# Optimization experiments

Hardware: AMD Instinct MI355X
Metric: run time of the kernel (lower is better)

The kernel has to match this reference:

```python
import jax, jax.numpy as jnp
import numpy as np

D_MODEL = 1024
NUM_HEADS = 16
D_K = D_MODEL // NUM_HEADS


def setup_inputs() -> dict:
    key = jax.random.key(0)
    ks = jax.random.split(key, 9)
    B, S = 2, 2048
    s = 1.0 / np.sqrt(D_MODEL)
    return {
        "x": jax.random.normal(ks[0], (B, S, D_MODEL), dtype=jnp.float32),
        "Wq": jax.random.normal(ks[1], (D_MODEL, D_MODEL), dtype=jnp.float32) * s,
        "bq": jnp.zeros((D_MODEL,), dtype=jnp.float32),
        "Wk": jax.random.normal(ks[2], (D_MODEL, D_MODEL), dtype=jnp.float32) * s,
        "bk": jnp.zeros((D_MODEL,), dtype=jnp.float32),
        "Wv": jax.random.normal(ks[3], (D_MODEL, D_MODEL), dtype=jnp.float32) * s,
        "bv": jnp.zeros((D_MODEL,), dtype=jnp.float32),
        "Wo": jax.random.normal(ks[4], (D_MODEL, D_MODEL), dtype=jnp.float32) * s,
        "bo": jnp.zeros((D_MODEL,), dtype=jnp.float32),
    }


def reference(x, Wq, bq, Wk, bk, Wv, bv, Wo, bo):
    B, S, _ = x.shape
    # project and split heads: [B, H, S, d_k]
    def proj(W, b):
        return (x @ W + b).reshape(B, S, NUM_HEADS, D_K).transpose(0, 2, 1, 3)
    Q, K, V = proj(Wq, bq), proj(Wk, bk), proj(Wv, bv)
    scores = jnp.einsum("bhqd,bhkd->bhqk", Q, K) / jnp.sqrt(jnp.float32(D_K))
    causal = jnp.tril(jnp.ones((S, S), dtype=bool))
    scores = jnp.where(causal[None, None], scores, jnp.float32(-1e9))
    attn = jax.nn.softmax(scores, axis=-1)  # dropout=0 (eval)
    out = jnp.einsum("bhqk,bhkd->bhqd", attn, V)
    out = out.transpose(0, 2, 1, 3).reshape(B, S, D_MODEL)
    return out @ Wo + bo
```

## Files before the change

kernel.cpp:

```cpp
#include <hip/hip_runtime.h>

#define SEQ    2048
#define NH     16
#define DMODEL 1024

typedef __attribute__((ext_vector_type(4)))  float f32x4;
typedef __attribute__((ext_vector_type(8)))  short s16x8;
typedef __attribute__((ext_vector_type(4)))  short s16x4;
typedef __attribute__((ext_vector_type(2)))  unsigned u32x2;

__device__ __forceinline__ float bf2f(unsigned short u){
  union { unsigned int i; float f; } v; v.i = ((unsigned int)u) << 16; return v.f;
}
__device__ __forceinline__ unsigned short f2bf(float f){
  union { float f; unsigned int i; } v; v.f = f;
  unsigned int r = v.i + 0x7fffu + ((v.i >> 16) & 1u);
  return (unsigned short)(r >> 16);
}
__device__ __forceinline__ unsigned short f2bf_hu(float f){
  union { float f; unsigned int i; } v; v.f = f;
  return (unsigned short)((v.i + 0x8000u) >> 16);
}
__device__ __forceinline__ float fast_exp2(float x){
  return __builtin_amdgcn_exp2f(x);
}
__device__ __forceinline__ void gld_lds16(const void* g, void* l){
  __builtin_amdgcn_global_load_lds((const __attribute__((address_space(1))) void*)g,
                                   (__attribute__((address_space(3))) void*)l,
                                   16, 0, 0);
}
#define SB() __builtin_amdgcn_sched_barrier(0)

__global__ __launch_bounds__(256) void k_prep(const float* __restrict__ x,
                                              const float* __restrict__ W0,
                                              const float* __restrict__ W1,
                                              const float* __restrict__ W2,
                                              const float* __restrict__ W3,
                                              unsigned short* __restrict__ Wt,
                                              unsigned short* __restrict__ xh){
  __shared__ float t[64][65];
  const int bid = blockIdx.x;
  const int tid = threadIdx.x;
  if (bid < 1024){
    const int z = bid >> 8, rem = bid & 255;
    const int n0 = (rem & 15) * 64, k0 = (rem >> 4) * 64;
    const float* Ws[4] = {W0, W1, W2, W3};
    const float* W = Ws[z];
    #pragma unroll
    for (int i = 0; i < 16; ++i){
      int e = i * 256 + tid;
      int r = e >> 6, c = e & 63;
      t[r][c] = W[(size_t)(k0 + r) * 1024 + n0 + c];
    }
    __syncthreads();
    size_t base = ((size_t)z << 20);
    #pragma unroll
    for (int i = 0; i < 16; ++i){
      int e = i * 256 + tid;
      int nn = e >> 6, kk = e & 63;
      Wt[base + (size_t)(n0 + nn) * 1024 + k0 + kk] = f2bf(t[kk][nn]);
    }
  } else {
    int i = (bid - 1024) * 256 + tid;
    f32x4 v = ((const f32x4*)x)[i];
    s16x4 h;
    #pragma unroll
    for (int j = 0; j < 4; ++j) h[j] = (short)f2bf(v[j]);
    ((s16x4*)xh)[i] = h;
  }
}

__global__ __launch_bounds__(512, 2)
void gemm_qkv8(const unsigned short* __restrict__ A,
               const unsigned short* __restrict__ B,
               const float* __restrict__ bq, const float* __restrict__ bk,
               const float* __restrict__ bv,
               unsigned short* __restrict__ Qb, unsigned short* __restrict__ Kb,
               unsigned short* __restrict__ Vt)
{
  __shared__ __align__(16) unsigned short lA[2][256 * 64];
  __shared__ __align__(16) unsigned short lB[2][192 * 64];
  const int tid = threadIdx.x;
  const int lane = tid & 63, w = tid >> 6;
  const int wm = w >> 2, wn = w & 3;
  const int lr = lane & 15, lq = lane >> 4;
  const int wg  = blockIdx.x + blockIdx.y * 16;
  const int swz = (wg & 7) * 32 + (wg >> 3);
  const int m0 = (swz >> 4) * 256, n0 = (swz & 15) * 192;

  size_t asrc[4]; unsigned adst[4];
  #pragma unroll
  for (int p = 0; p < 4; ++p){
    int c = p * 512 + tid;
    int row = c >> 3, lc = (c & 7) ^ (row & 7);
    asrc[p] = (size_t)(m0 + row) * 1024 + lc * 8;
    adst[p] = c * 8;
  }
  size_t bsrc[3]; unsigned bdst[3];
  #pragma unroll
  for (int p = 0; p < 3; ++p){
    int c = p * 512 + tid;
    int row = c >> 3, lc = (c & 7) ^ (row & 7);
    bsrc[p] = (size_t)(n0 + row) * 1024 + lc * 8;
    bdst[p] = c * 8;
  }
  auto stage = [&](int buf, int k0){
    #pragma unroll
    for (int p = 0; p < 4; ++p) gld_lds16(A + asrc[p] + k0, &lA[buf][adst[p]]);
    #pragma unroll
    for (int p = 0; p < 3; ++p) gld_lds16(B + bsrc[p] + k0, &lB[buf][bdst[p]]);
  };

  const int csw0 = ((0 + lq) ^ (lr & 7)) << 4;
  const int csw1 = ((4 + lq) ^ (lr & 7)) << 4;

  f32x4 acc[8][3];
  #pragma unroll
  for (int i = 0; i < 8; ++i)
    #pragma unroll
    for (int j = 0; j < 3; ++j) acc[i][j] = (f32x4)0.0f;

  stage(0, 0);
  stage(1, 64);
  asm volatile("s_waitcnt vmcnt(7)" ::: "memory");
  SB();
  __builtin_amdgcn_s_barrier();
  SB();

  for (int t = 0; t < 16; ++t){
    const int p = t & 1;
    s16x8 fa[8][2], fb[3][2];
    const char* baseA = (const char*)&lA[p][0];
    const char* baseB = (const char*)&lB[p][0];
    #pragma unroll
    for (int mf = 0; mf < 8; ++mf)
      fa[mf][0] = *(const s16x8*)(baseA + (wm * 128 + mf * 16 + lr) * 128 + csw0);
    #pragma unroll
    for (int nf = 0; nf < 3; ++nf)
      fb[nf][0] = *(const s16x8*)(baseB + (wn * 48 + nf * 16 + lr) * 128 + csw0);
    SB();
    #pragma unroll
    for (int mf = 0; mf < 8; ++mf)
      fa[mf][1] = *(const s16x8*)(baseA + (wm * 128 + mf * 16 + lr) * 128 + csw1);
    #pragma unroll
    for (int nf = 0; nf < 3; ++nf)
      fb[nf][1] = *(const s16x8*)(baseB + (wn * 48 + nf * 16 + lr) * 128 + csw1);
    asm volatile("s_waitcnt lgkmcnt(11)" ::: "memory");
    SB();
    #pragma unroll
    for (int mf = 0; mf < 8; ++mf)
      #pragma unroll
      for (int nf = 0; nf < 3; ++nf)
        acc[mf][nf] = __builtin_amdgcn_mfma_f32_16x16x32_bf16(fa[mf][0], fb[nf][0], acc[mf][nf], 0, 0, 0);
    SB();
    asm volatile("s_waitcnt lgkmcnt(0)" ::: "memory");
    SB();
    __builtin_amdgcn_s_barrier();
    SB();
    if (t + 2 < 16) stage(p, (t + 2) * 64);
    #pragma unroll
    for (int mf = 0; mf < 8; ++mf)
      #pragma unroll
      for (int nf = 0; nf < 3; ++nf)
        acc[mf][nf] = __builtin_amdgcn_mfma_f32_16x16x32_bf16(fa[mf][1], fb[nf][1], acc[mf][nf], 0, 0, 0);
    SB();
    if (t < 14) asm volatile("s_waitcnt vmcnt(7)" ::: "memory");
    else        asm volatile("s_waitcnt vmcnt(0)" ::: "memory");
    SB();
    __builtin_amdgcn_s_barrier();
    SB();
  }

  const int mb = m0 + wm * 128, nb = n0 + wn * 48;
  #pragma unroll
  for (int mf = 0; mf < 8; ++mf){
    int row = mb + mf * 16 + lq * 4;
    #pragma unroll
    for (int nf = 0; nf < 3; ++nf){
      int col = nb + nf * 16 + lr;
      int mat = col >> 10, cm = col & 1023;
      float bs = ((mat == 0) ? bq : (mat == 1) ? bk : bv)[cm];
      if (mat < 2){
        unsigned short* QK = mat ? Kb : Qb;
        #pragma unroll
        for (int r = 0; r < 4; ++r)
          QK[(size_t)(row + r) * 1024 + cm] = f2bf(acc[mf][nf][r] + bs);
      } else {
        int bb = row >> 11, s = row & 2047;
        int h = cm >> 6, d = cm & 63;
        s16x4 pk;
        #pragma unroll
        for (int r = 0; r < 4; ++r) pk[r] = (short)f2bf(acc[mf][nf][r] + bs);
        *(s16x4*)&Vt[(((size_t)(bb * NH + h) * 64 + d) << 11) + s] = pk;
      }
    }
  }
}

__global__ __launch_bounds__(256, 2)
void gemm_o8(const unsigned short* __restrict__ A,
             const unsigned short* __restrict__ B,
             const float* __restrict__ bias,
             float* __restrict__ C)
{
  __shared__ __align__(16) unsigned short lA[2][64 * 64];
  __shared__ __align__(16) unsigned short lB[2][128 * 64];
  const int tid = threadIdx.x;
  const int lane = tid & 63, w = tid >> 6;
  const int wm = w >> 1, wn = w & 1;
  const int lr = lane & 15, lq = lane >> 4;
  const int wg  = blockIdx.x + blockIdx.y * 8;
  const int swz = (wg & 7) * 64 + (wg >> 3);
  const int m0 = (swz >> 3) * 64, n0 = (swz & 7) * 128;

  size_t asrc[2]; unsigned adst[2];
  #pragma unroll
  for (int p = 0; p < 2; ++p){
    int c = p * 256 + tid;
    int row = c >> 3, lc = (c & 7) ^ (row & 7);
    asrc[p] = (size_t)(m0 + row) * 1024 + lc * 8;
    adst[p] = c * 8;
  }
  size_t bsrc[4]; unsigned bdst[4];
  #pragma unroll
  for (int p = 0; p < 4; ++p){
    int c = p * 256 + tid;
    int row = c >> 3, lc = (c & 7) ^ (row & 7);
    bsrc[p] = (size_t)(n0 + row) * 1024 + lc * 8;
    bdst[p] = c * 8;
  }
  auto stage = [&](int buf, int k0){
    #pragma unroll
    for (int p = 0; p < 2; ++p) gld_lds16(A + asrc[p] + k0, &lA[buf][adst[p]]);
    #pragma unroll
    for (int p = 0; p < 4; ++p) gld_lds16(B + bsrc[p] + k0, &lB[buf][bdst[p]]);
  };

  const int csw0 = ((0 + lq) ^ (lr & 7)) << 4;
  const int csw1 = ((4 + lq) ^ (lr & 7)) << 4;

  f32x4 acc[2][4];
  #pragma unroll
  for (int i = 0; i < 2; ++i)
    #pragma unroll
    for (int j = 0; j < 4; ++j) acc[i][j] = (f32x4)0.0f;

  stage(0, 0);
  stage(1, 64);
  asm volatile("s_waitcnt vmcnt(6)" ::: "memory");
  SB();
  __builtin_amdgcn_s_barrier();
  SB();

  for (int t = 0; t < 16; ++t){
    const int p = t & 1;
    s16x8 fa[2][2], fb[4][2];
    const char* baseA = (const char*)&lA[p][0];
    const char* baseB = (const char*)&lB[p][0];
    #pragma unroll
    for (int mf = 0; mf < 2; ++mf)
      fa[mf][0] = *(const s16x8*)(baseA + (wm * 32 + mf * 16 + lr) * 128 + csw0);
    #pragma unroll
    for (int nf = 0; nf < 4; ++nf)
      fb[nf][0] = *(const s16x8*)(baseB + (wn * 64 + nf * 16 + lr) * 128 + csw0);
    SB();
    #pragma unroll
    for (int mf = 0; mf < 2; ++mf)
      fa[mf][1] = *(const s16x8*)(baseA + (wm * 32 + mf * 16 + lr) * 128 + csw1);
    #pragma unroll
    for (int nf = 0; nf < 4; ++nf)
      fb[nf][1] = *(const s16x8*)(baseB + (wn * 64 + nf * 16 + lr) * 128 + csw1);
    asm volatile("s_waitcnt lgkmcnt(6)" ::: "memory");
    SB();
    #pragma unroll
    for (int i = 0; i < 2; ++i)
      #pragma unroll
      for (int j = 0; j < 4; ++j)
        acc[i][j] = __builtin_amdgcn_mfma_f32_16x16x32_bf16(fa[i][0], fb[j][0], acc[i][j], 0, 0, 0);
    SB();
    asm volatile("s_waitcnt lgkmcnt(0)" ::: "memory");
    SB();
    __builtin_amdgcn_s_barrier();
    SB();
    if (t + 2 < 16) stage(p, (t + 2) * 64);
    #pragma unroll
    for (int i = 0; i < 2; ++i)
      #pragma unroll
      for (int j = 0; j < 4; ++j)
        acc[i][j] = __builtin_amdgcn_mfma_f32_16x16x32_bf16(fa[i][1], fb[j][1], acc[i][j], 0, 0, 0);
    SB();
    if (t < 14) asm volatile("s_waitcnt vmcnt(6)" ::: "memory");
    else        asm volatile("s_waitcnt vmcnt(0)" ::: "memory");
    SB();
    __builtin_amdgcn_s_barrier();
    SB();
  }

  const int mb = m0 + wm * 32, nb = n0 + wn * 64;
  #pragma unroll
  for (int i = 0; i < 2; ++i){
    int row = mb + i * 16 + lq * 4;
    #pragma unroll
    for (int j = 0; j < 4; ++j){
      int col = nb + j * 16 + lr;
      float bs = bias[col];
      #pragma unroll
      for (int r = 0; r < 4; ++r)
        C[(size_t)(row + r) * 1024 + col] = acc[i][j][r] + bs;
    }
  }
}

__global__ __launch_bounds__(256, 4)
void attn_fwd(const unsigned short* __restrict__ Qg,
              const unsigned short* __restrict__ Kg,
              const unsigned short* __restrict__ Vtg,
              unsigned short* __restrict__ Oh)
{
  __shared__ __align__(16) unsigned short lK[2][64 * 64];
  __shared__ __align__(16) unsigned short lV[2][64 * 64];
  __shared__ __align__(16) unsigned short lP[4][16 * 64];
  const int tid = threadIdx.x;
  const int lane = tid & 63, w = tid >> 6;
  const int lr = lane & 15, lq = lane >> 4;
  const int bh = blockIdx.x;
  const int b = bh >> 4, h = bh & 15;
  const int qt = 31 - blockIdx.y;
  const int qrow = qt * 64 + w * 16;

  const float qscale = 0.125f * 1.44269504088896f;
  const float FIXMAX = 11.0f;

  const unsigned short* qp = Qg + (size_t)(b * SEQ + qrow + lr) * 1024 + h * 64 + lq * 8;
  s16x8 q0 = *(const s16x8*)qp;
  s16x8 q1 = *(const s16x8*)(qp + 32);
  #pragma unroll
  for (int j = 0; j < 8; ++j){
    q0[j] = (short)f2bf(bf2f((unsigned short)q0[j]) * qscale);
    q1[j] = (short)f2bf(bf2f((unsigned short)q1[j]) * qscale);
  }

  float ls = 0.f;
  f32x4 accO[4];
  #pragma unroll
  for (int dt = 0; dt < 4; ++dt) accO[dt] = (f32x4)0.0f;

  auto stage = [&](int buf, int kt){
    const int kc0 = kt * 64;
    #pragma unroll
    for (int it = 0; it < 2; ++it){
      int c = it * 256 + tid;
      int row = c >> 3, sc = c & 7;
      int lc = sc ^ (row & 7);
      gld_lds16(Kg + (size_t)(b * SEQ + kc0 + row) * 1024 + h * 64 + lc * 8, &lK[buf][c * 8]);
      gld_lds16(Vtg + ((size_t)(bh * 64 + row) << 11) + kc0 + lc * 8, &lV[buf][c * 8]);
    }
  };

  stage(0, 0);
  if (qt > 0){
    stage(1, 1);
    asm volatile("s_waitcnt vmcnt(4)" ::: "memory");
  } else {
    asm volatile("s_waitcnt vmcnt(0)" ::: "memory");
  }
  SB();
  __builtin_amdgcn_s_barrier();
  SB();

  for (int kt = 0; kt <= qt; ++kt){
    const int cur = kt & 1;
    const bool diag = (kt == qt);

    s16x8 kf[4][2], vf[4][2];
    #pragma unroll
    for (int st = 0; st < 4; ++st){
      int tok = st * 16 + lr;
      const char* kb = (const char*)&lK[cur][0] + tok * 128;
      kf[st][0] = *(const s16x8*)(kb + (((0 + lq) ^ (tok & 7)) << 4));
      kf[st][1] = *(const s16x8*)(kb + (((4 + lq) ^ (tok & 7)) << 4));
    }
    SB();
    #pragma unroll
    for (int st = 0; st < 4; ++st){
      int tok = st * 16 + lr;
      const char* vb = (const char*)&lV[cur][0] + tok * 128;
      vf[st][0] = *(const s16x8*)(vb + (((0 + lq) ^ (tok & 7)) << 4));
      vf[st][1] = *(const s16x8*)(vb + (((4 + lq) ^ (tok & 7)) << 4));
    }
    asm volatile("s_waitcnt lgkmcnt(8)" ::: "memory");
    SB();

    f32x4 s4[4];
    #pragma unroll
    for (int st = 0; st < 4; ++st){
      if (diag && st > w){ s4[st] = (f32x4)(-1e30f); continue; }
      f32x4 z = (f32x4)0.0f;
      z = __builtin_amdgcn_mfma_f32_16x16x32_bf16(kf[st][0], q0, z, 0, 0, 0);
      z = __builtin_amdgcn_mfma_f32_16x16x32_bf16(kf[st][1], q1, z, 0, 0, 0);
      if (diag && st == w){
        #pragma unroll
        for (int r = 0; r < 4; ++r)
          if (lq * 4 + r > lr) z[r] = -1e30f;
      }
      s4[st] = z;
    }
    SB();
    asm volatile("s_waitcnt lgkmcnt(0)" ::: "memory");
    SB();
    __builtin_amdgcn_s_barrier();
    SB();
    if (kt + 2 <= qt) stage(cur, kt + 2);

    char* pb = (char*)&lP[w][0];
    #pragma unroll
    for (int st = 0; st < 4; ++st){
      float p0 = fast_exp2(s4[st][0] - FIXMAX);
      float p1 = fast_exp2(s4[st][1] - FIXMAX);
      float p2 = fast_exp2(s4[st][2] - FIXMAX);
      float p3 = fast_exp2(s4[st][3] - FIXMAX);
      ls += (p0 + p1) + (p2 + p3);
      u32x2 d;
      d[0] = ((unsigned)f2bf_hu(p1) << 16) | f2bf_hu(p0);
      d[1] = ((unsigned)f2bf_hu(p3) << 16) | f2bf_hu(p2);
      int base = lr * 128 + ((st * 32 + lq * 8) ^ ((lr & 7) << 4));
      *(u32x2*)(pb + base) = d;
    }
    asm volatile("s_waitcnt lgkmcnt(0)" ::: "memory");
    SB();
    s16x8 pf0 = *(const s16x8*)(pb + lr * 128 + (((0 + lq) << 4) ^ ((lr & 7) << 4)));
    s16x8 pf1 = *(const s16x8*)(pb + lr * 128 + (((4 + lq) << 4) ^ ((lr & 7) << 4)));

    #pragma unroll
    for (int dt = 0; dt < 4; ++dt){
      accO[dt] = __builtin_amdgcn_mfma_f32_16x16x32_bf16(pf0, vf[dt][0], accO[dt], 0, 0, 0);
      accO[dt] = __builtin_amdgcn_mfma_f32_16x16x32_bf16(pf1, vf[dt][1], accO[dt], 0, 0, 0);
    }
    SB();
    if (kt + 2 <= qt)      asm volatile("s_waitcnt vmcnt(4)" ::: "memory");
    else if (kt + 1 <= qt) asm volatile("s_waitcnt vmcnt(0)" ::: "memory");
    SB();
    __builtin_amdgcn_s_barrier();
    SB();
  }

  float t = ls;
  t += __shfl_xor(t, 16);
  t += __shfl_xor(t, 32);
  #pragma unroll
  for (int r = 0; r < 4; ++r){
    float rn = 1.0f / __shfl(t, lq * 4 + r);
    #pragma unroll
    for (int dt = 0; dt < 4; ++dt){
      size_t off = (size_t)(b * SEQ + qrow + lq * 4 + r) * 1024 + h * 64 + dt * 16 + lr;
      Oh[off] = f2bf(accO[dt][r] * rn);
    }
  }
}

extern "C" void kernel_launch(void* const* d_in, const int* in_sizes, int n_in,
                              void* d_out, int out_size, void* d_ws, size_t ws_size,
                              hipStream_t stream){
  (void)in_sizes; (void)n_in; (void)out_size; (void)ws_size;
  const float* x  = (const float*)d_in[0];
  const float* Wq = (const float*)d_in[1];
  const float* bq = (const float*)d_in[2];
  const float* Wk = (const float*)d_in[3];
  const float* bk = (const float*)d_in[4];
  const float* Wv = (const float*)d_in[5];
  const float* bv = (const float*)d_in[6];
  const float* Wo = (const float*)d_in[7];
  const float* bo = (const float*)d_in[8];

  const size_t NT = 4096;
  unsigned short* xh  = (unsigned short*)d_ws;
  unsigned short* wt  = xh + NT * 1024;
  unsigned short* Qb  = wt + 4u * 1024 * 1024;
  unsigned short* Kb  = Qb + NT * 1024;
  unsigned short* Vt  = Kb + NT * 1024;
  unsigned short* Ohb = Vt + NT * 1024;

  k_prep<<<5120, 256, 0, stream>>>(x, Wq, Wk, Wv, Wo, wt, xh);

  gemm_qkv8<<<dim3(16, 16), 512, 0, stream>>>(xh, wt, bq, bk, bv, Qb, Kb, Vt);

  attn_fwd<<<dim3(32, 32), 256, 0, stream>>>(Qb, Kb, Vt, Ohb);

  const size_t WM = (size_t)1024 * 1024;
  gemm_o8<<<dim3(8, 64), 256, 0, stream>>>(Ohb, wt + 3 * WM, bo, (float*)d_out);
}
```

Before: 96.08 us.

## Split attention KV loop across wave pairs with 32-row query tiles

The attention kernel now uses 32-query-row tiles (twice as many blocks), and each pair of waves splits the KV tiles between them: one wave handles even tiles, the other odd tiles. The partial outputs and softmax sums are combined through LDS at the end. This aims to raise parallelism and shorten the causal critical path per block. In exchange it adds the cross-wave reduction, stages two KV tiles per iteration with a full vmcnt(0) wait (less prefetch overlap), and the odd-count last iteration leaves one wave idle.

After: 110.3 us. +14.8%, slower.

```diff
diff --git a/kernel.cpp b/kernel.cpp
--- a/kernel.cpp
+++ b/kernel.cpp
@@ -312,21 +312,25 @@
 }
 
 __global__ __launch_bounds__(256, 4)
-void attn_fwd(const unsigned short* __restrict__ Qg,
-              const unsigned short* __restrict__ Kg,
-              const unsigned short* __restrict__ Vtg,
-              unsigned short* __restrict__ Oh)
+void attn_fwd2(const unsigned short* __restrict__ Qg,
+               const unsigned short* __restrict__ Kg,
+               const unsigned short* __restrict__ Vtg,
+               unsigned short* __restrict__ Oh)
 {
   __shared__ __align__(16) unsigned short lK[2][64 * 64];
   __shared__ __align__(16) unsigned short lV[2][64 * 64];
   __shared__ __align__(16) unsigned short lP[4][16 * 64];
   const int tid = threadIdx.x;
   const int lane = tid & 63, w = tid >> 6;
+  const int rh = w >> 1, kp = w & 1;
   const int lr = lane & 15, lq = lane >> 4;
   const int bh = blockIdx.x;
   const int b = bh >> 4, h = bh & 15;
-  const int qt = 31 - blockIdx.y;
-  const int qrow = qt * 64 + w * 16;
+  const int qt = 63 - blockIdx.y;
+  const int qrow = qt * 32 + rh * 16;
+  const int nkv = (qt >> 1) + 1;
+  const int niter = (nkv + 1) >> 1;
+  const int qb16 = ((qt & 1) << 1) | rh;
 
   const float qscale = 0.125f * 1.44269504088896f;
   const float FIXMAX = 11.0f;
@@ -358,102 +362,112 @@
   };
 
   stage(0, 0);
-  if (qt > 0){
-    stage(1, 1);
-    asm volatile("s_waitcnt vmcnt(4)" ::: "memory");
-  } else {
-    asm volatile("s_waitcnt vmcnt(0)" ::: "memory");
-  }
+  if (nkv > 1) stage(1, 1);
+  asm volatile("s_waitcnt vmcnt(0)" ::: "memory");
   SB();
   __builtin_amdgcn_s_barrier();
   SB();
 
-  for (int kt = 0; kt <= qt; ++kt){
-    const int cur = kt & 1;
-    const bool diag = (kt == qt);
+  for (int j = 0; j < niter; ++j){
+    const int my_t = 2 * j + kp;
+    const bool active = (my_t < nkv);
+    const bool diag = (my_t == nkv - 1);
 
     s16x8 kf[4][2], vf[4][2];
-    #pragma unroll
-    for (int st = 0; st < 4; ++st){
-      int tok = st * 16 + lr;
-      const char* kb = (const char*)&lK[cur][0] + tok * 128;
-      kf[st][0] = *(const s16x8*)(kb + (((0 + lq) ^ (tok & 7)) << 4));
-      kf[st][1] = *(const s16x8*)(kb + (((4 + lq) ^ (tok & 7)) << 4));
-    }
-    SB();
-    #pragma unroll
-    for (int st = 0; st < 4; ++st){
-      int tok = st * 16 + lr;
-      const char* vb = (const char*)&lV[cur][0] + tok * 128;
-      vf[st][0] = *(const s16x8*)(vb + (((0 + lq) ^ (tok & 7)) << 4));
-      vf[st][1] = *(const s16x8*)(vb + (((4 + lq) ^ (tok & 7)) << 4));
-    }
-    asm volatile("s_waitcnt lgkmcnt(8)" ::: "memory");
-    SB();
-
-    f32x4 s4[4];
-    #pragma unroll
-    for (int st = 0; st < 4; ++st){
-      if (diag && st > w){ s4[st] = (f32x4)(-1e30f); continue; }
-      f32x4 z = (f32x4)0.0f;
-      z = __builtin_amdgcn_mfma_f32_16x16x32_bf16(kf[st][0], q0, z, 0, 0, 0);
-      z = __builtin_amdgcn_mfma_f32_16x16x32_bf16(kf[st][1], q1, z, 0, 0, 0);
-      if (diag && st == w){
-        #pragma unroll
-        for (int r = 0; r < 4; ++r)
-          if (lq * 4 + r > lr) z[r] = -1e30f;
+    if (active){
+      #pragma unroll
+      for (int st = 0; st < 4; ++st){
+        int tok = st * 16 + lr;
+        const char* kb = (const char*)&lK[kp][0] + tok * 128;
+        kf[st][0] = *(const s16x8*)(kb + (((0 + lq) ^ (tok & 7)) << 4));
+        kf[st][1] = *(const s16x8*)(kb + (((4 + lq) ^ (tok & 7)) << 4));
+        const char* vb = (const char*)&lV[kp][0] + tok * 128;
+        vf[st][0] = *(const s16x8*)(vb + (((0 + lq) ^ (tok & 7)) << 4));
+        vf[st][1] = *(const s16x8*)(vb + (((4 + lq) ^ (tok & 7)) << 4));
       }
-      s4[st] = z;
-    }
-    SB();
+    }
     asm volatile("s_waitcnt lgkmcnt(0)" ::: "memory");
     SB();
     __builtin_amdgcn_s_barrier();
     SB();
-    if (kt + 2 <= qt) stage(cur, kt + 2);
-
-    char* pb = (char*)&lP[w][0];
-    #pragma unroll
-    for (int st = 0; st < 4; ++st){
-      float p0 = fast_exp2(s4[st][0] - FIXMAX);
-      float p1 = fast_exp2(s4[st][1] - FIXMAX);
-      float p2 = fast_exp2(s4[st][2] - FIXMAX);
-      float p3 = fast_exp2(s4[st][3] - FIXMAX);
-      ls += (p0 + p1) + (p2 + p3);
-      u32x2 d;
-      d[0] = ((unsigned)f2bf_hu(p1) << 16) | f2bf_hu(p0);
-      d[1] = ((unsigned)f2bf_hu(p3) << 16) | f2bf_hu(p2);
-      int base = lr * 128 + ((st * 32 + lq * 8) ^ ((lr & 7) << 4));
-      *(u32x2*)(pb + base) = d;
-    }
-    asm volatile("s_waitcnt lgkmcnt(0)" ::: "memory");
-    SB();
-    s16x8 pf0 = *(const s16x8*)(pb + lr * 128 + (((0 + lq) << 4) ^ ((lr & 7) << 4)));
-    s16x8 pf1 = *(const s16x8*)(pb + lr * 128 + (((4 + lq) << 4) ^ ((lr & 7) << 4)));
-
-    #pragma unroll
-    for (int dt = 0; dt < 4; ++dt){
-      accO[dt] = __builtin_amdgcn_mfma_f32_16x16x32_bf16(pf0, vf[dt][0], accO[dt], 0, 0, 0);
-      accO[dt] = __builtin_amdgcn_mfma_f32_16x16x32_bf16(pf1, vf[dt][1], accO[dt], 0, 0, 0);
-    }
-    SB();
-    if (kt + 2 <= qt)      asm volatile("s_waitcnt vmcnt(4)" ::: "memory");
-    else if (kt + 1 <= qt) asm volatile("s_waitcnt vmcnt(0)" ::: "memory");
+    if (2 * j + 2 < nkv) stage(0, 2 * j + 2);
+    if (2 * j + 3 < nkv) stage(1, 2 * j + 3);
+
+    if (active){
+      f32x4 s4[4];
+      #pragma unroll
+      for (int st = 0; st < 4; ++st){
+        if (diag && st > qb16){ s4[st] = (f32x4)(-1e30f); continue; }
+        f32x4 z = (f32x4)0.0f;
+        z = __builtin_amdgcn_mfma_f32_16x16x32_bf16(kf[st][0], q0, z, 0, 0, 0);
+        z = __builtin_amdgcn_mfma_f32_16x16x32_bf16(kf[st][1], q1, z, 0, 0, 0);
+        if (diag && st == qb16){
+          #pragma unroll
+          for (int r = 0; r < 4; ++r)
+            if (lq * 4 + r > lr) z[r] = -1e30f;
+        }
+        s4[st] = z;
+      }
+
+      char* pb = (char*)&lP[w][0];
+      #pragma unroll
+      for (int st = 0; st < 4; ++st){
+        float p0 = fast_exp2(s4[st][0] - FIXMAX);
+        float p1 = fast_exp2(s4[st][1] - FIXMAX);
+        float p2 = fast_exp2(s4[st][2] - FIXMAX);
+        float p3 = fast_exp2(s4[st][3] - FIXMAX);
+        ls += (p0 + p1) + (p2 + p3);
+        u32x2 d;
+        d[0] = ((unsigned)f2bf_hu(p1) << 16) | f2bf_hu(p0);
+        d[1] = ((unsigned)f2bf_hu(p3) << 16) | f2bf_hu(p2);
+        int base = lr * 128 + ((st * 32 + lq * 8) ^ ((lr & 7) << 4));
+        *(u32x2*)(pb + base) = d;
+      }
+      asm volatile("s_waitcnt lgkmcnt(0)" ::: "memory");
+      SB();
+      s16x8 pf0 = *(const s16x8*)(pb + lr * 128 + (((0 + lq) << 4) ^ ((lr & 7) << 4)));
+      s16x8 pf1 = *(const s16x8*)(pb + lr * 128 + (((4 + lq) << 4) ^ ((lr & 7) << 4)));
+
+      #pragma unroll
+      for (int dt = 0; dt < 4; ++dt){
+        accO[dt] = __builtin_amdgcn_mfma_f32_16x16x32_bf16(pf0, vf[dt][0], accO[dt], 0, 0, 0);
+        accO[dt] = __builtin_amdgcn_mfma_f32_16x16x32_bf16(pf1, vf[dt][1], accO[dt], 0, 0, 0);
+      }
+    }
+    SB();
+    asm volatile("s_waitcnt vmcnt(0)" ::: "memory");
     SB();
     __builtin_amdgcn_s_barrier();
     SB();
   }
 
-  float t = ls;
-  t += __shfl_xor(t, 16);
-  t += __shfl_xor(t, 32);
-  #pragma unroll
-  for (int r = 0; r < 4; ++r){
-    float rn = 1.0f / __shfl(t, lq * 4 + r);
-    #pragma unroll
-    for (int dt = 0; dt < 4; ++dt){
-      size_t off = (size_t)(b * SEQ + qrow + lq * 4 + r) * 1024 + h * 64 + dt * 16 + lr;
-      Oh[off] = f2bf(accO[dt][r] * rn);
+  float* cb = (float*)&lK[0][0];
+  const int cbi = (rh * 64 + lane) * 17;
+  if (kp == 1){
+    #pragma unroll
+    for (int dt = 0; dt < 4; ++dt)
+      #pragma unroll
+      for (int r = 0; r < 4; ++r) cb[cbi + dt * 4 + r] = accO[dt][r];
+    cb[cbi + 16] = ls;
+  }
+  __syncthreads();
+  if (kp == 0){
+    ls += cb[cbi + 16];
+    #pragma unroll
+    for (int dt = 0; dt < 4; ++dt)
+      #pragma unroll
+      for (int r = 0; r < 4; ++r) accO[dt][r] += cb[cbi + dt * 4 + r];
+    float t = ls;
+    t += __shfl_xor(t, 16);
+    t += __shfl_xor(t, 32);
+    #pragma unroll
+    for (int r = 0; r < 4; ++r){
+      float rn = 1.0f / __shfl(t, lq * 4 + r);
+      #pragma unroll
+      for (int dt = 0; dt < 4; ++dt){
+        size_t off = (size_t)(b * SEQ + qrow + lq * 4 + r) * 1024 + h * 64 + dt * 16 + lr;
+        Oh[off] = f2bf(accO[dt][r] * rn);
+      }
     }
   }
 }
@@ -484,7 +498,7 @@
 
   gemm_qkv8<<<dim3(16, 16), 512, 0, stream>>>(xh, wt, bq, bk, bv, Qb, Kb, Vt);
 
-  attn_fwd<<<dim3(32, 32), 256, 0, stream>>>(Qb, Kb, Vt, Ohb);
+  attn_fwd2<<<dim3(32, 64), 256, 0, stream>>>(Qb, Kb, Vt, Ohb);
 
   const size_t WM = (size_t)1024 * 1024;
   gemm_o8<<<dim3(8, 64), 256, 0, stream>>>(Ohb, wt + 3 * WM, bo, (float*)d_out);
```
